# Performance work log

Hardware: AMD Instinct MI355X
Metric: run time of the kernel (lower is better)

The kernel has to match this reference:

```python
import jax, jax.numpy as jnp
import numpy as np

ALPHA = 0.5
TEMP = 0.1
TEMP2 = 0.05  # hardcoded in nt_xent_loss2
NUM_CLASSES = 10
EPS = 1e-12


def setup_inputs() -> dict:
    key = jax.random.key(0)
    k1, k2, k3 = jax.random.split(key, 3)
    B, D, C = 4096, 256, NUM_CLASSES
    cls_feats = jax.random.normal(k1, (B, D), dtype=jnp.float32)
    predicts = jax.random.normal(k2, (B, C), dtype=jnp.float32)
    targets = jax.random.randint(k3, (B,), 0, C)
    return {"cls_feats": cls_feats, "predicts": predicts, "targets": targets}


def _nt_xent_loss(feats, labels):
    B = feats.shape[0]
    eye = jnp.eye(B, dtype=bool)
    same = labels[:, None] == labels[None, :]
    mask = (same & ~eye).astype(feats.dtype)            # positives, no diagonal
    s = jnp.einsum('bd,cd->bc', feats, feats) / TEMP     # [B,B]
    s = jnp.where(eye, 0.0, s)                           # subtract diag_embed(diag)
    logits = s - jax.lax.stop_gradient(jnp.max(s, axis=1, keepdims=True))
    log_denom = jnp.log(jnp.sum(jnp.exp(logits), axis=1, keepdims=True) + EPS)
    log_prob = logits * mask - log_denom
    mask_sum = jnp.sum(mask, axis=1)
    mask_sum = jnp.where(mask_sum == 0, 1.0, mask_sum)
    pos_logits = jnp.sum(mask * log_prob, axis=1) / mask_sum
    return -jnp.mean(pos_logits)


def _nt_xent_loss2(feats, labels):
    B = feats.shape[0]
    eye = jnp.eye(B, dtype=bool)
    same = labels[:, None] == labels[None, :]
    mask = (same & ~eye).astype(feats.dtype)
    diff = ~same                                         # mask2 / different-label pairs
    S = (feats @ feats.T) / TEMP2                        # [B,B]
    val = jnp.where(diff, S, 0.0)                        # dot * different_label_mask

    # The torch loop body depends only on labels[i] -> compute once per class.
    def per_class(c):
        neg = labels != c                                # negatives of class c
        in_sub = neg[:, None] & neg[None, :]             # submatrix membership
        # row max over columns restricted to the negative set
        maxdot = jnp.max(jnp.where(neg[None, :], val, -jnp.inf), axis=1)  # [B]
        shifted = jnp.where(in_sub, val - maxdot[:, None], -jnp.inf)
        s_c = jnp.sum(jnp.exp(shifted))                  # exp_terms.sum()
        n_c = jnp.sum(jnp.where(in_sub, diff, False).astype(jnp.float32))
        return s_c, n_c

    sums, counts = jax.lax.map(jax.checkpoint(per_class), jnp.arange(NUM_CLASSES))
    x = sums[labels]                                     # [B] negtive_dot_negtive_sum
    negsum = counts[labels]                              # [B]
    all_zero = jnp.all(negsum == 0)
    x = jnp.where(all_zero, x, x / negsum)
    log_prob_row = -jnp.log(x + EPS)                     # constant across each row
    mask_sum = jnp.sum(mask, axis=1)
    mask_sum_safe = jnp.where(mask_sum == 0, 1.0, mask_sum)
    pos_logits = (mask_sum * log_prob_row) / mask_sum_safe
    return -jnp.mean(pos_logits)


def reference(cls_feats, predicts, targets):
    norm = jnp.maximum(jnp.linalg.norm(cls_feats, axis=-1, keepdims=True), EPS)
    feats = cls_feats / norm                             # F.normalize(dim=-1)
    logp = jax.nn.log_softmax(predicts, axis=-1)
    ce = -jnp.mean(jnp.take_along_axis(logp, targets[:, None], axis=1)[:, 0])
    cl = _nt_xent_loss(feats, targets)
    tl = _nt_xent_loss2(feats, targets)
    return (1.0 - ALPHA) * ce + ALPHA * cl + 0.5 * ALPHA * tl
```

## Files before the change

### kernel.cpp

```cpp
#include <hip/hip_runtime.h>
#include <math.h>

#define B 4096
#define D 256
#define NC 10
#define LDW 65
#define ZERO4 22528

typedef __attribute__((ext_vector_type(8))) short bf16x8;
typedef __attribute__((ext_vector_type(4))) float f32x4;

__device__ __forceinline__ unsigned short f2bf(float x) {
    unsigned int u = __float_as_uint(x);
    u += 0x7FFFu + ((u >> 16) & 1u);
    return (unsigned short)(u >> 16);
}

__global__ void prep_kernel(const float* __restrict__ feats, const float* __restrict__ pred,
                            const int* __restrict__ tg, unsigned short* __restrict__ fN,
                            float4* __restrict__ bigz, int* __restrict__ h,
                            float* __restrict__ scal) {
    __shared__ int histL[16];
    const int t = threadIdx.x, w = t >> 6, l = t & 63;
    const int gid = t >> 4, lg = t & 15;
    const int r0 = blockIdx.x * 16;
    if (t < 16) histL[t] = 0;
    __syncthreads();
    int zi = blockIdx.x * 256 + t;
    if (zi < ZERO4) bigz[zi] = (float4){0.f, 0.f, 0.f, 0.f};

    int row = r0 + gid;
    float4 v[4];
#pragma unroll
    for (int k = 0; k < 4; k++) v[k] = ((const float4*)feats)[row * 64 + lg * 4 + k];
    float ss = 0.f;
#pragma unroll
    for (int k = 0; k < 4; k++)
        ss += v[k].x * v[k].x + v[k].y * v[k].y + v[k].z * v[k].z + v[k].w * v[k].w;
#pragma unroll
    for (int o = 1; o < 16; o <<= 1) ss += __shfl_xor(ss, o);
    float inv = 1.0f / fmaxf(sqrtf(ss), 1e-12f);
    bf16x8 o0, o1;
#pragma unroll
    for (int k = 0; k < 4; k++) {
        const float* vp = (const float*)&v[k];
        if (k < 2) {
#pragma unroll
            for (int e = 0; e < 4; e++) o0[k * 4 + e] = (short)f2bf(vp[e] * inv);
        } else {
#pragma unroll
            for (int e = 0; e < 4; e++) o1[(k - 2) * 4 + e] = (short)f2bf(vp[e] * inv);
        }
    }
    ((bf16x8*)fN)[row * 32 + lg * 2 + 0] = o0;
    ((bf16x8*)fN)[row * 32 + lg * 2 + 1] = o1;

    if (w == 0 && l < 16) atomicAdd(&histL[tg[r0 + l]], 1);
    if (w == 1 && l < 16) {
        const float* p = pred + (r0 + l) * NC;
        float m = p[0];
#pragma unroll
        for (int c = 1; c < NC; c++) m = fmaxf(m, p[c]);
        float s = 0.f;
#pragma unroll
        for (int c = 0; c < NC; c++) s += __expf(p[c] - m);
        float vce = m + logf(s) - p[tg[r0 + l]];
#pragma unroll
        for (int o = 1; o < 16; o <<= 1) vce += __shfl_xor(vce, o);
        if (l == 0) atomicAdd(&scal[0], vce);
    }
    __syncthreads();
    if (t < NC && histL[t]) atomicAdd(&h[t], histL[t]);
}

__global__ void scatter_kernel(const int* __restrict__ tg, const int* __restrict__ h,
                               int* __restrict__ ccnt, int* __restrict__ labelP,
                               int* __restrict__ origIdx, int* __restrict__ posOf) {
    __shared__ int cb[16];
    __shared__ int wcnt[4][16];
    __shared__ int wabs[4][16];
    const int t = threadIdx.x, w = t >> 6, l = t & 63;
    const int row = blockIdx.x * 256 + t;
    const int c = tg[row];
    if (t == 0) {
        int s = 0;
        for (int cc = 0; cc < NC; cc++) { cb[cc] = s; s += h[cc]; }
    }
    unsigned long long below = (l == 0) ? 0ull : ((~0ull) >> (64 - l));
    int rank = 0;
#pragma unroll
    for (int cc = 0; cc < NC; cc++) {
        unsigned long long m = __ballot(c == cc);
        if (c == cc) rank = __popcll(m & below);
        if (l == 0) wcnt[w][cc] = __popcll(m);
    }
    __syncthreads();
    if (t < NC) {
        int pre[4], s = 0;
#pragma unroll
        for (int ww = 0; ww < 4; ww++) { pre[ww] = s; s += wcnt[ww][t]; }
        int b = cb[t] + atomicAdd(&ccnt[t], s);
#pragma unroll
        for (int ww = 0; ww < 4; ww++) wabs[ww][t] = b + pre[ww];
    }
    __syncthreads();
    int pos = wabs[w][c] + rank;
    labelP[pos] = c;
    origIdx[pos] = row;
    posOf[row] = pos;
}

__launch_bounds__(256)
__global__ void gemm_kernel(const unsigned short* __restrict__ fN,
                            const int* __restrict__ tg, const int* __restrict__ labelP,
                            const int* __restrict__ origIdx, const int* __restrict__ posOf,
                            float* __restrict__ E1, float* __restrict__ P1,
                            float* __restrict__ E2G, int* __restrict__ M2K) {
    __shared__ float scW[4][16 * LDW];
    __shared__ int labS[256];
    __shared__ float E2L[32 * 11];
    __shared__ int M2L[32 * 11];
    __shared__ float E1L[32], P1L[32];

    const int t = threadIdx.x;
    const int w = t >> 6, l = t & 63;
    const int qr = l >> 4, lm = l & 15;
    const int row0 = blockIdx.x * 32;
    const int colB = blockIdx.y * 256;

    labS[t] = labelP[colB + t];
    for (int s = t; s < 32 * 11; s += 256) { E2L[s] = 0.f; M2L[s] = 0; }
    if (t < 32) { E1L[t] = 0.f; P1L[t] = 0.f; }

    int offB[4];
#pragma unroll
    for (int nb = 0; nb < 4; nb++)
        offB[nb] = origIdx[colB + w * 64 + nb * 16 + lm] * D + qr * 8;

    int liR[2], posR[2];
#pragma unroll
    for (int mb = 0; mb < 2; mb++) {
        int rg = row0 + mb * 16 + lm;
        liR[mb] = tg[rg];
        posR[mb] = posOf[rg];
    }

    const unsigned short* pa = fN + (row0 + lm) * D + qr * 8;

    f32x4 acc[2][4];
#pragma unroll
    for (int mb = 0; mb < 2; mb++)
#pragma unroll
        for (int nb = 0; nb < 4; nb++) acc[mb][nb] = (f32x4){0.f, 0.f, 0.f, 0.f};

#pragma unroll 2
    for (int ks = 0; ks < 8; ks++) {
        bf16x8 af[2], bfr[4];
#pragma unroll
        for (int mb = 0; mb < 2; mb++) af[mb] = *(const bf16x8*)(pa + mb * 16 * D + ks * 32);
#pragma unroll
        for (int nb = 0; nb < 4; nb++) bfr[nb] = *(const bf16x8*)(fN + offB[nb] + ks * 32);
#pragma unroll
        for (int mb = 0; mb < 2; mb++)
#pragma unroll
            for (int nb = 0; nb < 4; nb++)
                acc[mb][nb] = __builtin_amdgcn_mfma_f32_16x16x32_bf16(af[mb], bfr[nb],
                                                                      acc[mb][nb], 0, 0, 0);
    }
    __syncthreads();

#pragma unroll
    for (int mb = 0; mb < 2; mb++) {
#pragma unroll
        for (int nb = 0; nb < 4; nb++)
#pragma unroll
            for (int r = 0; r < 4; r++)
                scW[w][(qr * 4 + r) * LDW + nb * 16 + lm] = acc[mb][nb][r];
        const int rowL = mb * 16 + lm;
        const int li = liR[mb];
        const int posr = posR[mb];
        const float* srow = &scW[w][lm * LDW + qr * 16];
        const int colg0 = colB + w * 64 + qr * 16;
        float e1sumA = 0.f, e1sumB = 0.f, p1sum = 0.f;
        int seg = -1; float segEA = 0.f, segEB = 0.f; int segK = 0;
#pragma unroll
        for (int j = 0; j < 16; j++) {
            float g = srow[j];
            int lj = labS[w * 64 + qr * 16 + j];
            bool diag = (colg0 + j == posr);
            bool same = (lj == li);
            float s1 = diag ? 0.f : 10.f * g;
            float e1 = __expf(s1);
            if (j & 1) e1sumB += e1; else e1sumA += e1;
            p1sum += (same && !diag) ? s1 : 0.f;
            if (lj != seg) {
                if (seg >= 0) {
                    float segE = segEA + segEB;
                    if (segE > 0.f) atomicAdd(&E2L[rowL * 11 + seg], segE);
                    if (segK > 0) atomicMax(&M2L[rowL * 11 + seg], segK);
                }
                seg = lj; segEA = 0.f; segEB = 0.f; segK = 0;
            }
            if (!same) {
                if (j & 1) segEB += e1 * e1; else segEA += e1 * e1;
                segK = max(segK, __float_as_int(20.f * g + 64.f));
            }
        }
        if (seg >= 0) {
            float segE = segEA + segEB;
            if (segE > 0.f) atomicAdd(&E2L[rowL * 11 + seg], segE);
            if (segK > 0) atomicMax(&M2L[rowL * 11 + seg], segK);
        }
        float e1sum = e1sumA + e1sumB;
        e1sum += __shfl_xor(e1sum, 16); e1sum += __shfl_xor(e1sum, 32);
        p1sum += __shfl_xor(p1sum, 16); p1sum += __shfl_xor(p1sum, 32);
        if (qr == 0) {
            atomicAdd(&E1L[rowL], e1sum);
            atomicAdd(&P1L[rowL], p1sum);
        }
    }
    __syncthreads();

    if (t < 32) {
        atomicAdd(&E1[row0 + t], E1L[t]);
        atomicAdd(&P1[row0 + t], P1L[t]);
    }
    for (int s = t; s < 32 * NC; s += 256) {
        int r = s / NC, c = s - r * NC;
        float e = E2L[r * 11 + c];
        int k = M2L[r * 11 + c];
        if (e > 0.f) atomicAdd(&E2G[(row0 + r) * NC + c], e);
        if (k > 0) atomicMax(&M2K[(row0 + r) * NC + c], k);
    }
}

__global__ void rowfin_kernel(const int* __restrict__ tg, const int* __restrict__ h,
                              const float* __restrict__ E1, const float* __restrict__ P1,
                              const float* __restrict__ E2G, const int* __restrict__ M2K,
                              float* __restrict__ sums, float* __restrict__ scal,
                              int* __restrict__ done, float* __restrict__ out) {
    __shared__ float ssumL[16];
    __shared__ int lastS;
    const int t = threadIdx.x;
    if (t < 16) ssumL[t] = 0.f;
    __syncthreads();
    const int i = blockIdx.x * 64 + t;
    const int li = tg[i];
    float E2[NC], M2[NC];
#pragma unroll
    for (int k = 0; k < NC; k++) {
        E2[k] = E2G[i * NC + k];
        int key = M2K[i * NC + k];
        M2[k] = (key > 0) ? (__int_as_float(key) - 64.f) : -3.0e38f;
    }
    const int hl = h[li];
    E2[li] = (float)hl;
    M2[li] = 0.f;
    float m1 = -3.0e38f, m2 = -3.0e38f;
    int a1 = -1;
#pragma unroll
    for (int k = 0; k < NC; k++) {
        float v = M2[k];
        if (v > m1) { m2 = m1; m1 = v; a1 = k; }
        else if (v > m2) m2 = v;
    }
    float Es = 0.f;
#pragma unroll
    for (int k = 0; k < NC; k++) Es += E2[k];
#pragma unroll
    for (int c = 0; c < NC; c++) {
        if (c == li) continue;
        float T = Es - E2[c];
        if (T > 0.f) {
            float md = (a1 == c) ? m2 : m1;
            atomicAdd(&ssumL[c], __expf(-md) * T);
        }
    }
    float cn = (float)(hl - 1);
    float pos1 = (cn > 0.f) ? (P1[i] / cn - logf(E1[i])) : 0.f;
#pragma unroll
    for (int o = 1; o < 64; o <<= 1) pos1 += __shfl_xor(pos1, o);
    if (t == 0) atomicAdd(&scal[1], pos1);
    __syncthreads();
    if (t < NC && ssumL[t] > 0.f) atomicAdd(&sums[t], ssumL[t]);

    __threadfence();
    if (t == 0) lastS = (atomicAdd(done, 1) == 63);
    __syncthreads();
    if (lastS && t == 0) {
        int hh[NC];
        long long S2 = 0;
        for (int c = 0; c < NC; c++) { hh[c] = h[c]; S2 += (long long)hh[c] * hh[c]; }
        float ncs[NC];
        int az = 1;
        for (int c = 0; c < NC; c++) {
            long long M = (long long)B - hh[c];
            long long n = M * M - (S2 - (long long)hh[c] * hh[c]);
            ncs[c] = (float)n;
            if (hh[c] > 0 && n != 0) az = 0;
        }
        float possum = 0.f;
        for (int c = 0; c < NC; c++) {
            if (hh[c] > 1) {
                float x = atomicAdd(&sums[c], 0.f);
                if (!az) x = x / ncs[c];
                possum += (float)hh[c] * (-logf(x + 1e-12f));
            }
        }
        float ce = scal[0] / (float)B;
        float cl = -(atomicAdd(&scal[1], 0.f) / (float)B);
        float tl = -(possum / (float)B);
        float loss = 0.5f * ce + 0.5f * cl + 0.25f * tl;
        unsigned int bits = __float_as_uint(loss);
        unsigned int hedged = (bits & 0xFFFF0000u) | (bits >> 16);
        *(unsigned int*)out = hedged;
    }
}

extern "C" void kernel_launch(void* const* d_in, const int* in_sizes, int n_in,
                              void* d_out, int out_size, void* d_ws, size_t ws_size,
                              hipStream_t stream) {
    (void)in_sizes; (void)n_in; (void)out_size; (void)ws_size;
    const float* feats = (const float*)d_in[0];
    const float* pred = (const float*)d_in[1];
    const int* tg = (const int*)d_in[2];
    float* out = (float*)d_out;

    unsigned short* fN = (unsigned short*)d_ws;
    float* E1 = (float*)(fN + B * D);
    float* P1 = E1 + B;
    float* E2G = P1 + B;
    int* M2K = (int*)(E2G + B * NC);
    int* h = M2K + B * NC;
    int* ccnt = h + 16;
    float* sums = (float*)(ccnt + 16);
    float* scal = sums + 16;
    int* done = (int*)(scal + 16);
    int* labelP = done + 16;
    int* origIdx = labelP + B;
    int* posOf = origIdx + B;

    hipMemsetAsync(h, 0, 5 * 16 * sizeof(int), stream);

    prep_kernel<<<B / 16, 256, 0, stream>>>(feats, pred, tg, fN, (float4*)E1, h, scal);
    scatter_kernel<<<B / 256, 256, 0, stream>>>(tg, h, ccnt, labelP, origIdx, posOf);
    gemm_kernel<<<dim3(B / 32, B / 256), 256, 0, stream>>>(fN, tg, labelP, origIdx, posOf,
                                                           E1, P1, E2G, M2K);
    rowfin_kernel<<<B / 64, 64, 0, stream>>>(tg, h, E1, P1, E2G, M2K, sums, scal, done, out);
}
```

Measured before the change: 142.8 us.

## Normalize features into label-sorted order and drop index indirection in GEMM

Feature normalization and bf16 conversion move into the scatter kernel, which writes rows directly at their label-sorted positions. The GEMM then reads both operands contiguously from the sorted buffer and uses sorted labels, removing the origIdx/posOf gathers. The per-segment E2/M2 accumulation no longer masks same-label columns, relying on rowfin overwriting that class entry, and atomics become unconditional. The risk is that normalization now runs on only 16 blocks, which may serialize memory traffic.

```diff
diff --git a/kernel.cpp b/kernel.cpp
--- a/kernel.cpp
+++ b/kernel.cpp
@@ -16,44 +16,16 @@
     return (unsigned short)(u >> 16);
 }
 
-__global__ void prep_kernel(const float* __restrict__ feats, const float* __restrict__ pred,
-                            const int* __restrict__ tg, unsigned short* __restrict__ fN,
+__global__ void prep_kernel(const float* __restrict__ pred, const int* __restrict__ tg,
                             float4* __restrict__ bigz, int* __restrict__ h,
                             float* __restrict__ scal) {
     __shared__ int histL[16];
     const int t = threadIdx.x, w = t >> 6, l = t & 63;
-    const int gid = t >> 4, lg = t & 15;
     const int r0 = blockIdx.x * 16;
     if (t < 16) histL[t] = 0;
     __syncthreads();
     int zi = blockIdx.x * 256 + t;
     if (zi < ZERO4) bigz[zi] = (float4){0.f, 0.f, 0.f, 0.f};
-
-    int row = r0 + gid;
-    float4 v[4];
-#pragma unroll
-    for (int k = 0; k < 4; k++) v[k] = ((const float4*)feats)[row * 64 + lg * 4 + k];
-    float ss = 0.f;
-#pragma unroll
-    for (int k = 0; k < 4; k++)
-        ss += v[k].x * v[k].x + v[k].y * v[k].y + v[k].z * v[k].z + v[k].w * v[k].w;
-#pragma unroll
-    for (int o = 1; o < 16; o <<= 1) ss += __shfl_xor(ss, o);
-    float inv = 1.0f / fmaxf(sqrtf(ss), 1e-12f);
-    bf16x8 o0, o1;
-#pragma unroll
-    for (int k = 0; k < 4; k++) {
-        const float* vp = (const float*)&v[k];
-        if (k < 2) {
-#pragma unroll
-            for (int e = 0; e < 4; e++) o0[k * 4 + e] = (short)f2bf(vp[e] * inv);
-        } else {
-#pragma unroll
-            for (int e = 0; e < 4; e++) o1[(k - 2) * 4 + e] = (short)f2bf(vp[e] * inv);
-        }
-    }
-    ((bf16x8*)fN)[row * 32 + lg * 2 + 0] = o0;
-    ((bf16x8*)fN)[row * 32 + lg * 2 + 1] = o1;
 
     if (w == 0 && l < 16) atomicAdd(&histL[tg[r0 + l]], 1);
     if (w == 1 && l < 16) {
@@ -73,14 +45,16 @@
     if (t < NC && histL[t]) atomicAdd(&h[t], histL[t]);
 }
 
-__global__ void scatter_kernel(const int* __restrict__ tg, const int* __restrict__ h,
-                               int* __restrict__ ccnt, int* __restrict__ labelP,
-                               int* __restrict__ origIdx, int* __restrict__ posOf) {
+__global__ void scatter_kernel(const float* __restrict__ feats, const int* __restrict__ tg,
+                               const int* __restrict__ h, int* __restrict__ ccnt,
+                               int* __restrict__ labelP, unsigned short* __restrict__ fP) {
     __shared__ int cb[16];
     __shared__ int wcnt[4][16];
     __shared__ int wabs[4][16];
+    __shared__ int posS[256];
     const int t = threadIdx.x, w = t >> 6, l = t & 63;
-    const int row = blockIdx.x * 256 + t;
+    const int r0 = blockIdx.x * 256;
+    const int row = r0 + t;
     const int c = tg[row];
     if (t == 0) {
         int s = 0;
@@ -106,14 +80,44 @@
     __syncthreads();
     int pos = wabs[w][c] + rank;
     labelP[pos] = c;
-    origIdx[pos] = row;
-    posOf[row] = pos;
+    posS[t] = pos;
+    __syncthreads();
+
+    const int gid = t >> 4, lg = t & 15;
+#pragma unroll 4
+    for (int it = 0; it < 16; ++it) {
+        const int r = it * 16 + gid;
+        float4 v[4];
+#pragma unroll
+        for (int k = 0; k < 4; k++) v[k] = ((const float4*)feats)[(r0 + r) * 64 + lg * 4 + k];
+        float ss = 0.f;
+#pragma unroll
+        for (int k = 0; k < 4; k++)
+            ss += v[k].x * v[k].x + v[k].y * v[k].y + v[k].z * v[k].z + v[k].w * v[k].w;
+#pragma unroll
+        for (int o = 1; o < 16; o <<= 1) ss += __shfl_xor(ss, o);
+        float inv = 1.0f / fmaxf(sqrtf(ss), 1e-12f);
+        bf16x8 o0, o1;
+#pragma unroll
+        for (int k = 0; k < 4; k++) {
+            const float* vp = (const float*)&v[k];
+            if (k < 2) {
+#pragma unroll
+                for (int e = 0; e < 4; e++) o0[k * 4 + e] = (short)f2bf(vp[e] * inv);
+            } else {
+#pragma unroll
+                for (int e = 0; e < 4; e++) o1[(k - 2) * 4 + e] = (short)f2bf(vp[e] * inv);
+            }
+        }
+        const int dst = posS[r];
+        ((bf16x8*)fP)[dst * 32 + lg * 2 + 0] = o0;
+        ((bf16x8*)fP)[dst * 32 + lg * 2 + 1] = o1;
+    }
 }
 
 __launch_bounds__(256)
-__global__ void gemm_kernel(const unsigned short* __restrict__ fN,
-                            const int* __restrict__ tg, const int* __restrict__ labelP,
-                            const int* __restrict__ origIdx, const int* __restrict__ posOf,
+__global__ void gemm_kernel(const unsigned short* __restrict__ fP,
+                            const int* __restrict__ labP,
                             float* __restrict__ E1, float* __restrict__ P1,
                             float* __restrict__ E2G, int* __restrict__ M2K) {
     __shared__ float scW[4][16 * LDW];
@@ -128,24 +132,16 @@
     const int row0 = blockIdx.x * 32;
     const int colB = blockIdx.y * 256;
 
-    labS[t] = labelP[colB + t];
+    labS[t] = labP[colB + t];
     for (int s = t; s < 32 * 11; s += 256) { E2L[s] = 0.f; M2L[s] = 0; }
     if (t < 32) { E1L[t] = 0.f; P1L[t] = 0.f; }
 
-    int offB[4];
-#pragma unroll
-    for (int nb = 0; nb < 4; nb++)
-        offB[nb] = origIdx[colB + w * 64 + nb * 16 + lm] * D + qr * 8;
-
-    int liR[2], posR[2];
-#pragma unroll
-    for (int mb = 0; mb < 2; mb++) {
-        int rg = row0 + mb * 16 + lm;
-        liR[mb] = tg[rg];
-        posR[mb] = posOf[rg];
-    }
-
-    const unsigned short* pa = fN + (row0 + lm) * D + qr * 8;
+    int liR[2];
+#pragma unroll
+    for (int mb = 0; mb < 2; mb++) liR[mb] = labP[row0 + mb * 16 + lm];
+
+    const unsigned short* pa = fP + (row0 + lm) * D + qr * 8;
+    const unsigned short* pb = fP + (colB + w * 64 + lm) * D + qr * 8;
 
     f32x4 acc[2][4];
 #pragma unroll
@@ -159,7 +155,7 @@
 #pragma unroll
         for (int mb = 0; mb < 2; mb++) af[mb] = *(const bf16x8*)(pa + mb * 16 * D + ks * 32);
 #pragma unroll
-        for (int nb = 0; nb < 4; nb++) bfr[nb] = *(const bf16x8*)(fN + offB[nb] + ks * 32);
+        for (int nb = 0; nb < 4; nb++) bfr[nb] = *(const bf16x8*)(pb + nb * 16 * D + ks * 32);
 #pragma unroll
         for (int mb = 0; mb < 2; mb++)
 #pragma unroll
@@ -178,7 +174,7 @@
                 scW[w][(qr * 4 + r) * LDW + nb * 16 + lm] = acc[mb][nb][r];
         const int rowL = mb * 16 + lm;
         const int li = liR[mb];
-        const int posr = posR[mb];
+        const int rg = row0 + mb * 16 + lm;
         const float* srow = &scW[w][lm * LDW + qr * 16];
         const int colg0 = colB + w * 64 + qr * 16;
         float e1sumA = 0.f, e1sumB = 0.f, p1sum = 0.f;
@@ -187,30 +183,23 @@
         for (int j = 0; j < 16; j++) {
             float g = srow[j];
             int lj = labS[w * 64 + qr * 16 + j];
-            bool diag = (colg0 + j == posr);
-            bool same = (lj == li);
+            bool diag = (colg0 + j == rg);
             float s1 = diag ? 0.f : 10.f * g;
             float e1 = __expf(s1);
             if (j & 1) e1sumB += e1; else e1sumA += e1;
-            p1sum += (same && !diag) ? s1 : 0.f;
+            p1sum += (lj == li && !diag) ? s1 : 0.f;
             if (lj != seg) {
                 if (seg >= 0) {
-                    float segE = segEA + segEB;
-                    if (segE > 0.f) atomicAdd(&E2L[rowL * 11 + seg], segE);
-                    if (segK > 0) atomicMax(&M2L[rowL * 11 + seg], segK);
+                    atomicAdd(&E2L[rowL * 11 + seg], segEA + segEB);
+                    atomicMax(&M2L[rowL * 11 + seg], segK);
                 }
                 seg = lj; segEA = 0.f; segEB = 0.f; segK = 0;
             }
-            if (!same) {
-                if (j & 1) segEB += e1 * e1; else segEA += e1 * e1;
-                segK = max(segK, __float_as_int(20.f * g + 64.f));
-            }
-        }
-        if (seg >= 0) {
-            float segE = segEA + segEB;
-            if (segE > 0.f) atomicAdd(&E2L[rowL * 11 + seg], segE);
-            if (segK > 0) atomicMax(&M2L[rowL * 11 + seg], segK);
-        }
+            if (j & 1) segEB += e1 * e1; else segEA += e1 * e1;
+            segK = max(segK, __float_as_int(20.f * g + 64.f));
+        }
+        atomicAdd(&E2L[rowL * 11 + seg], segEA + segEB);
+        atomicMax(&M2L[rowL * 11 + seg], segK);
         float e1sum = e1sumA + e1sumB;
         e1sum += __shfl_xor(e1sum, 16); e1sum += __shfl_xor(e1sum, 32);
         p1sum += __shfl_xor(p1sum, 16); p1sum += __shfl_xor(p1sum, 32);
@@ -234,7 +223,7 @@
     }
 }
 
-__global__ void rowfin_kernel(const int* __restrict__ tg, const int* __restrict__ h,
+__global__ void rowfin_kernel(const int* __restrict__ labP, const int* __restrict__ h,
                               const float* __restrict__ E1, const float* __restrict__ P1,
                               const float* __restrict__ E2G, const int* __restrict__ M2K,
                               float* __restrict__ sums, float* __restrict__ scal,
@@ -245,7 +234,7 @@
     if (t < 16) ssumL[t] = 0.f;
     __syncthreads();
     const int i = blockIdx.x * 64 + t;
-    const int li = tg[i];
+    const int li = labP[i];
     float E2[NC], M2[NC];
 #pragma unroll
     for (int k = 0; k < NC; k++) {
@@ -326,8 +315,8 @@
     const int* tg = (const int*)d_in[2];
     float* out = (float*)d_out;
 
-    unsigned short* fN = (unsigned short*)d_ws;
-    float* E1 = (float*)(fN + B * D);
+    unsigned short* fP = (unsigned short*)d_ws;
+    float* E1 = (float*)(fP + B * D);
     float* P1 = E1 + B;
     float* E2G = P1 + B;
     int* M2K = (int*)(E2G + B * NC);
@@ -337,14 +326,11 @@
     float* scal = sums + 16;
     int* done = (int*)(scal + 16);
     int* labelP = done + 16;
-    int* origIdx = labelP + B;
-    int* posOf = origIdx + B;
 
     hipMemsetAsync(h, 0, 5 * 16 * sizeof(int), stream);
 
-    prep_kernel<<<B / 16, 256, 0, stream>>>(feats, pred, tg, fN, (float4*)E1, h, scal);
-    scatter_kernel<<<B / 256, 256, 0, stream>>>(tg, h, ccnt, labelP, origIdx, posOf);
-    gemm_kernel<<<dim3(B / 32, B / 256), 256, 0, stream>>>(fN, tg, labelP, origIdx, posOf,
-                                                           E1, P1, E2G, M2K);
-    rowfin_kernel<<<B / 64, 64, 0, stream>>>(tg, h, E1, P1, E2G, M2K, sums, scal, done, out);
-}
+    prep_kernel<<<B / 16, 256, 0, stream>>>(pred, tg, (float4*)E1, h, scal);
+    scatter_kernel<<<B / 256, 256, 0, stream>>>(feats, tg, h, ccnt, labelP, fP);
+    gemm_kernel<<<dim3(B / 32, B / 256), 256, 0, stream>>>(fP, labelP, E1, P1, E2G, M2K);
+    rowfin_kernel<<<B / 64, 64, 0, stream>>>(labelP, h, E1, P1, E2G, M2K, sums, scal, done, out);
+}
```

New measurement: 154.2 us. 8.0% more time.
